# Kernel optimization log

Hardware: AMD Instinct MI355X
Metric: run time of the kernel (lower is better)

Reference implementation:

```python
import jax, jax.numpy as jnp
import numpy as np

B, C, H, W = 8, 512, 56, 56
CI = C // 2  # inter_channels
EPS = 1e-5   # BatchNorm eps


def setup_inputs() -> dict:
    key = jax.random.key(0)
    ks = jax.random.split(key, 11)
    s = 0.02
    return {
        "x": jax.random.normal(ks[0], (B, C, H, W), jnp.float32),
        "theta_w": jax.random.normal(ks[1], (CI, C), jnp.float32) * s,
        "theta_b": jnp.zeros((CI,), jnp.float32),
        "phi_w": jax.random.normal(ks[2], (CI, C), jnp.float32) * s,
        "phi_b": jnp.zeros((CI,), jnp.float32),
        "g_w": jax.random.normal(ks[3], (CI, C), jnp.float32) * s,
        "g_b": jnp.zeros((CI,), jnp.float32),
        "w_w": jax.random.normal(ks[4], (C, CI), jnp.float32) * s,
        "w_b": jnp.zeros((C,), jnp.float32),
        "bn_gamma": jax.random.normal(ks[5], (C,), jnp.float32) * 0.1,
        "bn_beta": jax.random.normal(ks[6], (C,), jnp.float32) * 0.1,
    }


def reference(x, theta_w, theta_b, phi_w, phi_b, g_w, g_b, w_w, w_b, bn_gamma, bn_beta):
    b, c, h, w = x.shape
    n = h * w

    def proj(wt, bi):  # 1x1 conv -> [b, out, n]
        return (jnp.einsum('bchw,oc->bohw', x, wt) + bi[None, :, None, None]).reshape(b, -1, n)

    theta_x = proj(theta_w, theta_b).transpose(0, 2, 1)  # [b, n, ci]
    phi_x = proj(phi_w, phi_b)                           # [b, ci, n]
    g_x = proj(g_w, g_b).transpose(0, 2, 1)             # [b, n, ci]

    f = jnp.einsum('bnc,bcm->bnm', theta_x, phi_x)       # [b, n, n] unscaled scores
    f_div_c = jax.nn.softmax(f, axis=-1)
    y = jnp.einsum('bnm,bmc->bnc', f_div_c, g_x)         # [b, n, ci]
    y = y.transpose(0, 2, 1).reshape(b, -1, h, w)        # [b, ci, h, w]

    w_y = jnp.einsum('bchw,oc->bohw', y, w_w) + w_b[None, :, None, None]
    # BatchNorm2d (training mode, batch statistics over B,H,W per channel)
    mean = w_y.mean(axis=(0, 2, 3))
    var = w_y.var(axis=(0, 2, 3))
    w_y = (w_y - mean[None, :, None, None]) * jax.lax.rsqrt(var[None, :, None, None] + EPS)
    w_y = w_y * bn_gamma[None, :, None, None] + bn_beta[None, :, None, None]
    return w_y + x
```

## Files before the change

kernel.cpp:

```cpp
#include <hip/hip_runtime.h>
#include <hip/hip_bf16.h>


typedef unsigned short u16;
typedef unsigned int u32;
typedef __attribute__((ext_vector_type(8))) short short8;
typedef __attribute__((ext_vector_type(4))) float floatx4;

#define B_   8
#define C_   512
#define CI_  256
#define N_   3136
#define BN_  25088

__device__ __forceinline__ u16 f2b(float f) {
    return __builtin_bit_cast(u16, __float2bfloat16(f));
}
__device__ __forceinline__ float b2f(u16 u) {
    return __bfloat162float(__builtin_bit_cast(__hip_bfloat16, u));
}
__device__ __forceinline__ floatx4 mfma16(short8 a, short8 b, floatx4 c) {
    return __builtin_amdgcn_mfma_f32_16x16x32_bf16(a, b, c, 0, 0, 0);
}
__device__ __forceinline__ void gload_lds16(const u16* g, u16* l) {
    __builtin_amdgcn_global_load_lds(
        (const __attribute__((address_space(1))) u32*)g,
        (__attribute__((address_space(3))) u32*)l, 16, 0, 0);
}

__device__ __forceinline__ int block_flag(const void* x) {
    __shared__ int cnt_;
    if (threadIdx.x == 0) cnt_ = 0;
    __syncthreads();
    const u32* xw = (const u32*)x;
    int c = 0;
#pragma unroll
    for (int i = 0; i < 4; ++i) {
        u32 w = xw[threadIdx.x * 4 + i];
        u32 e = (w >> 7) & 0xFF;
        c += (e >= 118 && e <= 130) ? 1 : 0;
    }
    atomicAdd(&cnt_, c);
    __syncthreads();
    return (2 * cnt_ > 1024) ? 1 : 0;
}

__global__ __launch_bounds__(256) void convert_params(
    const void* __restrict__ x,
    const void* tw, const void* tb, const void* pw, const void* pb,
    const void* gw, const void* gbi, const void* ww, const void* wb,
    const void* gamma, const void* beta,
    u16* __restrict__ dst, float* __restrict__ stats)
{
    const int fl = block_flag(x);
    if (blockIdx.x == 0 && blockIdx.y == 0) {
        stats[threadIdx.x] = 0.f;
        stats[threadIdx.x + 256] = 0.f;
        stats[threadIdx.x + 512] = 0.f;
        stats[threadIdx.x + 768] = 0.f;
    }
    const void* srcs[10] = {tw, tb, pw, pb, gw, gbi, ww, wb, gamma, beta};
    const int ns[10] = {131072, 256, 131072, 256, 131072, 256, 131072, 512, 512, 512};
    int seg = blockIdx.y;
    int off = 0;
    for (int s = 0; s < 10; ++s) { if (s == seg) break; off += ns[s]; }
    const void* src = srcs[seg];
    int n = ns[seg];
    int i0 = (blockIdx.x * 256 + threadIdx.x) * 8;
    if (i0 >= n) return;
    u16* d = dst + off;
    for (int k = 0; k < 8; ++k) {
        int i = i0 + k;
        if (i < n)
            d[i] = fl ? ((const u16*)src)[i] : f2b(((const float*)src)[i]);
    }
}

__global__ __launch_bounds__(256) void transpose_x(
    const void* __restrict__ in, u16* __restrict__ out)
{
    const int fl = block_flag(in);
    __shared__ u16 tile[64][68];
    const int t = threadIdx.x;
    const long base = (long)blockIdx.z * (long)C_ * (long)N_;
    const int c0 = blockIdx.x * 64, r0 = blockIdx.y * 64;
    const int lr = t >> 3;
    const int lc = (t & 7) * 8;
#pragma unroll
    for (int j = 0; j < 2; ++j) {
        int rr = lr + 32 * j;
        long eoff = base + (long)(r0 + rr) * N_ + c0 + lc;
        u16 v[8] __attribute__((aligned(16)));
        if (fl) {
            const u16* pi = (const u16*)in + eoff;
            *(uint64_t*)&v[0] = *(const uint64_t*)pi;
            *(uint64_t*)&v[4] = *(const uint64_t*)(pi + 4);
        } else {
            const float* pi = (const float*)in + eoff;
            floatx4 a = *(const floatx4*)pi;
            floatx4 b4 = *(const floatx4*)(pi + 4);
#pragma unroll
            for (int k = 0; k < 4; ++k) { v[k] = f2b(a[k]); v[4 + k] = f2b(b4[k]); }
        }
        *(uint64_t*)&tile[rr][lc] = *(const uint64_t*)&v[0];
        *(uint64_t*)&tile[rr][lc + 4] = *(const uint64_t*)&v[4];
    }
    __syncthreads();
#pragma unroll
    for (int j = 0; j < 2; ++j) {
        int oc = lr + 32 * j;
        int ob = (t & 7) * 8;
        u16 vals[8] __attribute__((aligned(16)));
#pragma unroll
        for (int k = 0; k < 8; ++k) vals[k] = tile[ob + k][oc];
        u16* po = out + (long)blockIdx.z * N_ * C_ + (long)(c0 + oc) * C_ + r0 + ob;
        *(uint64_t*)po = *(const uint64_t*)vals;
        *(uint64_t*)(po + 4) = *(const uint64_t*)(vals + 4);
    }
}

__global__ __launch_bounds__(256, 3) void gemm_proj(
    const u16* __restrict__ A,
    const u16* __restrict__ BtBase,
    u16* __restrict__ OutBase,
    u16* __restrict__ gT,
    long ostride)
{
    __shared__ __attribute__((aligned(16))) u16 smem[16896];
    const int t = threadIdx.x;
    const int wave = t >> 6, lane = t & 63;
    const int q = lane >> 4, lx = lane & 15;
    const int m0 = blockIdx.x * 128;
    const int n0 = blockIdx.y * 128;
    const int zz = blockIdx.z;
    const u16* Bt = BtBase + (long)zz * 131328L;
    const u16* bias = Bt + 131072;

    auto As = [&](int buf, int rg) -> u16* { return smem + (buf * 8 + rg) * 512; };
    auto Bs = [&](int buf, int rg) -> u16* { return smem + 8192 + (buf * 8 + rg) * 512; };

    floatx4 zero4 = {0.f, 0.f, 0.f, 0.f};
    floatx4 acc[4][4];
#pragma unroll
    for (int i = 0; i < 4; ++i)
#pragma unroll
        for (int j = 0; j < 4; ++j) acc[i][j] = zero4;

    auto stage = [&](int buf, int k0) {
#pragma unroll
        for (int i = 0; i < 2; ++i) {
            int rg = wave * 2 + i;
            gload_lds16(A + (long)(m0 + rg * 16 + lx) * C_ + k0 + q * 8, As(buf, rg));
            gload_lds16(Bt + (long)(n0 + rg * 16 + lx) * C_ + k0 + q * 8, Bs(buf, rg));
        }
    };

    stage(0, 0);
    const int rg0 = (wave >> 1) * 4, cg0 = (wave & 1) * 4;
    for (int s = 0; s < C_ / 32; ++s) {
        const int buf = s & 1;
        __syncthreads();
        if (s + 1 < C_ / 32) stage(buf ^ 1, (s + 1) * 32);
        short8 af[4], bfr[4];
#pragma unroll
        for (int i = 0; i < 4; ++i)
            af[i] = *(const short8*)(As(buf, rg0 + i) + lane * 8);
#pragma unroll
        for (int j = 0; j < 4; ++j)
            bfr[j] = *(const short8*)(Bs(buf, cg0 + j) + lane * 8);
#pragma unroll
        for (int i = 0; i < 4; ++i)
#pragma unroll
            for (int j = 0; j < 4; ++j)
                acc[i][j] = mfma16(af[i], bfr[j], acc[i][j]);
    }

    const int wr = (wave >> 1) * 64, wc = (wave & 1) * 64;
    if (zz < 2) {
        u16* Out = OutBase + (long)zz * ostride;
#pragma unroll
        for (int j = 0; j < 4; ++j) {
            int col = n0 + wc + j * 16 + lx;
            float bv = b2f(bias[col]);
#pragma unroll
            for (int i = 0; i < 4; ++i)
#pragma unroll
                for (int r = 0; r < 4; ++r) {
                    int row = m0 + wr + i * 16 + q * 4 + r;
                    Out[(long)row * CI_ + col] = f2b(acc[i][j][r] + bv);
                }
        }
    } else {
        __syncthreads();
#pragma unroll
        for (int j = 0; j < 4; ++j) {
            int cl = wc + j * 16 + lx;
            float bv = b2f(bias[n0 + cl]);
#pragma unroll
            for (int i = 0; i < 4; ++i)
#pragma unroll
                for (int r = 0; r < 4; ++r)
                    smem[cl * 132 + wr + i * 16 + q * 4 + r] =
                        f2b(acc[i][j][r] + bv);
        }
        __syncthreads();
#pragma unroll
        for (int p = 0; p < 4; ++p) {
            int cc = (t >> 3) + p * 32;
            int nn0 = (t & 7) * 16;
            u16 vals[16] __attribute__((aligned(16)));
#pragma unroll
            for (int k = 0; k < 16; ++k) vals[k] = smem[cc * 132 + nn0 + k];
            int m = m0 + nn0;
            int bb = m / N_;
            int nn = m - bb * N_;
            u16* dst = gT + ((long)bb * CI_ + (n0 + cc)) * N_ + nn;
            *(short8*)dst = *(const short8*)&vals[0];
            *(short8*)(dst + 8) = *(const short8*)&vals[8];
        }
    }
}

__global__ __launch_bounds__(256, 2) void attn(
    const u16* __restrict__ theta,
    const u16* __restrict__ phi,
    const u16* __restrict__ gT,
    u16* __restrict__ yp0, u16* __restrict__ yp1,
    u16* __restrict__ yp2, u16* __restrict__ yp3,
    float* __restrict__ lpart)
{
    __shared__ __attribute__((aligned(16))) u16 psf[2][8][2][64][8];
    __shared__ __attribute__((aligned(16))) u16 gsf[2][16][64][8];
    __shared__ __attribute__((aligned(16))) u16 Ps[4][32][40];

    const int t = threadIdx.x;
    const int wave = t >> 6, lane = t & 63;
    const int q = lane >> 4, lx = lane & 15;
    const int b = blockIdx.y;
    const int z = blockIdx.z;
    const int n0w = blockIdx.x * 128 + wave * 32;
    const bool valid = n0w < N_;
    const u16* thb = theta + (long)b * N_ * CI_;
    const u16* phb = phi + (long)b * N_ * CI_;
    const u16* gb = gT + (long)b * CI_ * N_;

    short8 tf[2][8];
#pragma unroll
    for (int h = 0; h < 2; ++h) {
        int trow = n0w + h * 16 + lx;
        if (trow >= N_) trow = N_ - 1;
#pragma unroll
        for (int kk = 0; kk < 8; ++kk)
            tf[h][kk] = *(const short8*)(thb + (long)trow * CI_ + kk * 32 + q * 8);
    }

    floatx4 zero4 = {0.f, 0.f, 0.f, 0.f};
    floatx4 yacc[2][16];
#pragma unroll
    for (int h = 0; h < 2; ++h)
#pragma unroll
        for (int i = 0; i < 16; ++i) yacc[h][i] = zero4;
    floatx4 lacc[2] = {zero4, zero4};
    const short8 ones = {0x3F80, 0x3F80, 0x3F80, 0x3F80,
                         0x3F80, 0x3F80, 0x3F80, 0x3F80};

    const int mbeg = z * 800;
    const int mend = (z == 3) ? N_ : mbeg + 800;

    auto stage = [&](int buf, int m0) {
#pragma unroll
        for (int i = 0; i < 2; ++i) {
            int kc = wave * 2 + i;
#pragma unroll
            for (int h = 0; h < 2; ++h)
                gload_lds16(phb + (long)(m0 + h * 16 + lx) * CI_ + kc * 32 + q * 8,
                            &psf[buf][kc][h][0][0]);
        }
#pragma unroll
        for (int j4 = 0; j4 < 4; ++j4) {
            int ct = wave * 4 + j4;
            gload_lds16(gb + (long)(ct * 16 + lx) * N_ + m0 + q * 8,
                        &gsf[buf][ct][0][0]);
        }
    };

    stage(0, mbeg);
    const int NSTEP = (mend - mbeg) / 32;
    for (int s = 0; s < NSTEP; ++s) {
        const int buf = s & 1;
        __syncthreads();
        if (s + 1 < NSTEP) stage(buf ^ 1, mbeg + (s + 1) * 32);

        floatx4 sacc[2][2];
        sacc[0][0] = zero4; sacc[0][1] = zero4;
        sacc[1][0] = zero4; sacc[1][1] = zero4;
#pragma unroll
        for (int kk = 0; kk < 8; ++kk) {
            short8 bf0 = *(const short8*)&psf[buf][kk][0][lane][0];
            short8 bf1 = *(const short8*)&psf[buf][kk][1][lane][0];
            sacc[0][0] = mfma16(tf[0][kk], bf0, sacc[0][0]);
            sacc[1][0] = mfma16(tf[1][kk], bf0, sacc[1][0]);
            sacc[0][1] = mfma16(tf[0][kk], bf1, sacc[0][1]);
            sacc[1][1] = mfma16(tf[1][kk], bf1, sacc[1][1]);
        }

#pragma unroll
        for (int h = 0; h < 2; ++h)
#pragma unroll
            for (int mh = 0; mh < 2; ++mh)
#pragma unroll
                for (int r = 0; r < 4; ++r) {
                    float e = __expf(fminf(sacc[h][mh][r], 60.f));
                    Ps[wave][h * 16 + q * 4 + r][mh * 16 + lx] = f2b(e);
                }
        short8 gpre[4];
#pragma unroll
        for (int j = 0; j < 4; ++j)
            gpre[j] = *(const short8*)&gsf[buf][j][lane][0];
        __builtin_amdgcn_wave_barrier();
        short8 pA0 = *(const short8*)&Ps[wave][lx][q * 8];
        short8 pA1 = *(const short8*)&Ps[wave][16 + lx][q * 8];
        __builtin_amdgcn_wave_barrier();

#pragma unroll
        for (int j = 0; j < 4; ++j) {
            yacc[0][j] = mfma16(pA0, gpre[j], yacc[0][j]);
            yacc[1][j] = mfma16(pA1, gpre[j], yacc[1][j]);
        }
#pragma unroll
        for (int ct = 4; ct < 16; ++ct) {
            short8 gf = *(const short8*)&gsf[buf][ct][lane][0];
            yacc[0][ct] = mfma16(pA0, gf, yacc[0][ct]);
            yacc[1][ct] = mfma16(pA1, gf, yacc[1][ct]);
        }
        lacc[0] = mfma16(pA0, ones, lacc[0]);
        lacc[1] = mfma16(pA1, ones, lacc[1]);
    }

    if (valid) {
        u16* ypz = (z == 0) ? yp0 : (z == 1) ? yp1 : (z == 2) ? yp2 : yp3;
        u16* yb = ypz + (long)b * N_ * CI_;
#pragma unroll
        for (int h = 0; h < 2; ++h)
#pragma unroll
            for (int ct = 0; ct < 16; ++ct)
#pragma unroll
                for (int r = 0; r < 4; ++r)
                    yb[(long)(n0w + h * 16 + q * 4 + r) * CI_ + ct * 16 + lx] =
                        f2b(yacc[h][ct][r]);
        if (lx == 0) {
#pragma unroll
            for (int h = 0; h < 2; ++h)
#pragma unroll
                for (int r = 0; r < 4; ++r)
                    lpart[(long)z * BN_ + (long)b * N_ + n0w + h * 16 + q * 4 + r] =
                        lacc[h][r];
        }
    }
}

__global__ __launch_bounds__(256, 3) void gemm_w(
    const u16* __restrict__ yp0, const u16* __restrict__ yp1,
    const u16* __restrict__ yp2, const u16* __restrict__ yp3,
    const float* __restrict__ lpart,
    const u16* __restrict__ Bt,
    const u16* __restrict__ bias,
    u16* __restrict__ wy,
    float* __restrict__ stats)
{
    __shared__ __attribute__((aligned(16))) u16 Asf[2][8][64][8];
    __shared__ __attribute__((aligned(16))) u16 Bsf[2][8][64][8];

    const int t = threadIdx.x;
    const int wave = t >> 6, lane = t & 63;
    const int q = lane >> 4, lx = lane & 15;
    const int m0 = blockIdx.x * 128;
    const int n0 = blockIdx.y * 128;

    float rl[2];
#pragma unroll
    for (int i = 0; i < 2; ++i) {
        int row = m0 + (wave * 2 + i) * 16 + lx;
        rl[i] = 1.0f / (lpart[row] + lpart[BN_ + row] +
                        lpart[2 * BN_ + row] + lpart[3 * BN_ + row]);
    }

    floatx4 zero4 = {0.f, 0.f, 0.f, 0.f};
    floatx4 acc[4][4];
#pragma unroll
    for (int i = 0; i < 4; ++i)
#pragma unroll
        for (int j = 0; j < 4; ++j) acc[i][j] = zero4;

    short8 va[2][4];
    auto loadA = [&](int k0) {
#pragma unroll
        for (int i = 0; i < 2; ++i) {
            long off = (long)(m0 + (wave * 2 + i) * 16 + lx) * CI_ + k0 + q * 8;
            va[i][0] = *(const short8*)(yp0 + off);
            va[i][1] = *(const short8*)(yp1 + off);
            va[i][2] = *(const short8*)(yp2 + off);
            va[i][3] = *(const short8*)(yp3 + off);
        }
    };
    auto writeA = [&](int buf) {
#pragma unroll
        for (int i = 0; i < 2; ++i) {
            u16 pk[8] __attribute__((aligned(16)));
#pragma unroll
            for (int e = 0; e < 8; ++e) {
                float v = (b2f(((const u16*)&va[i][0])[e]) +
                           b2f(((const u16*)&va[i][1])[e]) +
                           b2f(((const u16*)&va[i][2])[e]) +
                           b2f(((const u16*)&va[i][3])[e])) * rl[i];
                pk[e] = f2b(v);
            }
            *(short8*)&Asf[buf][wave * 2 + i][lane][0] = *(const short8*)pk;
        }
    };
    auto stageB = [&](int buf, int k0) {
#pragma unroll
        for (int i = 0; i < 2; ++i) {
            int rg = wave * 2 + i;
            gload_lds16(Bt + (long)(n0 + rg * 16 + lx) * CI_ + k0 + q * 8,
                        &Bsf[buf][rg][0][0]);
        }
    };

    loadA(0); writeA(0); stageB(0, 0);
    const int rg0 = (wave >> 1) * 4, cg0 = (wave & 1) * 4;
    const int NS = CI_ / 32;
    for (int s = 0; s < NS; ++s) {
        const int buf = s & 1;
        __syncthreads();
        if (s + 1 < NS) { loadA((s + 1) * 32); stageB(buf ^ 1, (s + 1) * 32); }
        short8 af[4], bfr[4];
#pragma unroll
        for (int i = 0; i < 4; ++i)
            af[i] = *(const short8*)&Asf[buf][rg0 + i][lane][0];
#pragma unroll
        for (int j = 0; j < 4; ++j)
            bfr[j] = *(const short8*)&Bsf[buf][cg0 + j][lane][0];
#pragma unroll
        for (int i = 0; i < 4; ++i)
#pragma unroll
            for (int j = 0; j < 4; ++j)
                acc[i][j] = mfma16(af[i], bfr[j], acc[i][j]);
        if (s + 1 < NS) writeA(buf ^ 1);
    }

    const int wr = (wave >> 1) * 64, wc = (wave & 1) * 64;
#pragma unroll
    for (int j = 0; j < 4; ++j) {
        int col = n0 + wc + j * 16 + lx;
        float bv = b2f(bias[col]);
        float cs = 0.f, cq = 0.f;
#pragma unroll
        for (int i = 0; i < 4; ++i)
#pragma unroll
            for (int r = 0; r < 4; ++r) {
                int row = m0 + wr + i * 16 + q * 4 + r;
                float v = acc[i][j][r] + bv;
                wy[(long)row * C_ + col] = f2b(v);
                cs += v; cq += v * v;
            }
        cs += __shfl_xor(cs, 16); cs += __shfl_xor(cs, 32);
        cq += __shfl_xor(cq, 16); cq += __shfl_xor(cq, 32);
        if (q == 0) {
            atomicAdd(&stats[col], cs);
            atomicAdd(&stats[C_ + col], cq);
        }
    }
}

__global__ __launch_bounds__(256) void bn_apply(
    const u16* __restrict__ wy, const void* __restrict__ xv,
    const u16* __restrict__ gamma, const u16* __restrict__ beta,
    const float* __restrict__ stats, void* __restrict__ outv)
{
    const int fl = block_flag(xv);
    __shared__ float tile[64][65];
    const int t = threadIdx.x;
    const int nb0 = blockIdx.x * 64;
    const int c0 = blockIdx.y * 64;
    const int b = blockIdx.z;
#pragma unroll
    for (int j = 0; j < 4; ++j) {
        int row = (t >> 4) + 16 * j;
        int col = (t & 15) * 4;
        const u16* p = wy + ((long)b * N_ + nb0 + row) * C_ + c0 + col;
        u16 lv[4] __attribute__((aligned(8)));
        *(uint64_t*)lv = *(const uint64_t*)p;
#pragma unroll
        for (int k = 0; k < 4; ++k) tile[row][col + k] = b2f(lv[k]);
    }
    __syncthreads();
    const float inv = 1.0f / (float)BN_;
#pragma unroll
    for (int it = 0; it < 8; ++it) {
        int oc = (t >> 5) + 8 * it;
        int on = (t & 31) * 2;
        int c = c0 + oc;
        float mean = stats[c] * inv;
        float var = stats[C_ + c] * inv - mean * mean;
        float rstd = rsqrtf(var + 1e-5f);
        float sc = b2f(gamma[c]) * rstd;
        float sh = b2f(beta[c]) - mean * sc;
        long base = ((long)b * C_ + c) * N_ + nb0 + on;
        float v0 = tile[on][oc] * sc + sh;
        float v1 = tile[on + 1][oc] * sc + sh;
        if (fl) {
            v0 += b2f(((const u16*)xv)[base]);
            v1 += b2f(((const u16*)xv)[base + 1]);
            ((u16*)outv)[base] = f2b(v0);
            ((u16*)outv)[base + 1] = f2b(v1);
        } else {
            v0 += ((const float*)xv)[base];
            v1 += ((const float*)xv)[base + 1];
            ((float*)outv)[base] = v0;
            ((float*)outv)[base + 1] = v1;
        }
    }
}

extern "C" void kernel_launch(void* const* d_in, const int* in_sizes, int n_in,
                              void* d_out, int out_size, void* d_ws, size_t ws_size,
                              hipStream_t stream)
{
    (void)in_sizes; (void)n_in; (void)out_size; (void)ws_size;

    const size_t S = 12845056;
    const size_t SE = S / 2;
    char* base = (char*)d_ws;
    u16*   xT    = (u16*)(base);
    u16*   yp3   = (u16*)(base);
    u16*   yp2   = (u16*)(base + S);
    u16*   th    = (u16*)(base + 2 * S);
    u16*   wy    = (u16*)(base + 2 * S);
    u16*   gT    = (u16*)(base + 4 * S);
    float* lpart = (float*)(base + 5 * S);
    float* stats = (float*)(base + 5 * S + (size_t)4 * BN_ * 4);
    u16*   cw    = (u16*)(base + 5 * S + (size_t)4 * BN_ * 4 + 4096);

    u16* ctw = cw;
    u16* cww = cw + 393984;
    u16* cwb = cw + 525056;
    u16* cga = cw + 525568;
    u16* cbe = cw + 526080;

    u16* yp0 = (u16*)d_out;
    u16* yp1 = (u16*)d_out + SE;

    convert_params<<<dim3(64, 10), 256, 0, stream>>>(
        d_in[0], d_in[1], d_in[2], d_in[3], d_in[4], d_in[5], d_in[6],
        d_in[7], d_in[8], d_in[9], d_in[10], cw, stats);

    transpose_x<<<dim3(N_ / 64, C_ / 64, B_), 256, 0, stream>>>(d_in[0], xT);

    gemm_proj<<<dim3(BN_ / 128, CI_ / 128, 3), 256, 0, stream>>>(
        xT, ctw, th, gT, (long)SE);

    attn<<<dim3(25, B_, 4), 256, 0, stream>>>(
        th, th + SE, gT, yp0, yp1, yp2, yp3, lpart);

    gemm_w<<<dim3(BN_ / 128, C_ / 128), 256, 0, stream>>>(
        yp0, yp1, yp2, yp3, lpart, cww, cwb, wy, stats);

    bn_apply<<<dim3(N_ / 64, C_ / 64, B_), 256, 0, stream>>>(
        wy, d_in[0], cga, cbe, stats, d_out);
}
```

Baseline: 375.1 us.

## Transpose softmax tile in registers via permlane swaps instead of LDS round-trip

Swaps the MFMA operand order so the score accumulator comes out transposed, then packs the exponentials to bf16 with v_cvt_pk_bf16_f32 and rearranges them across lanes with v_permlane32/16_swap. This produces the A-operand for the P·G MFMA directly in registers, removing the per-wave LDS scratch buffer, its writes and reads, and the wave barriers. It also raises wave priority around the MFMA blocks with s_setprio. The lane permutation must exactly match the MFMA operand layout, so the change depends on CDNA-specific instructions.

```diff
diff --git a/kernel.cpp b/kernel.cpp
--- a/kernel.cpp
+++ b/kernel.cpp
@@ -6,6 +6,7 @@
 typedef unsigned int u32;
 typedef __attribute__((ext_vector_type(8))) short short8;
 typedef __attribute__((ext_vector_type(4))) float floatx4;
+typedef __attribute__((ext_vector_type(4))) u32 uint4v;
 
 #define B_   8
 #define C_   512
@@ -231,7 +232,6 @@
 {
     __shared__ __attribute__((aligned(16))) u16 psf[2][8][2][64][8];
     __shared__ __attribute__((aligned(16))) u16 gsf[2][16][64][8];
-    __shared__ __attribute__((aligned(16))) u16 Ps[4][32][40];
 
     const int t = threadIdx.x;
     const int wave = t >> 6, lane = t & 63;
@@ -294,47 +294,53 @@
         floatx4 sacc[2][2];
         sacc[0][0] = zero4; sacc[0][1] = zero4;
         sacc[1][0] = zero4; sacc[1][1] = zero4;
+        __builtin_amdgcn_s_setprio(1);
 #pragma unroll
         for (int kk = 0; kk < 8; ++kk) {
             short8 bf0 = *(const short8*)&psf[buf][kk][0][lane][0];
             short8 bf1 = *(const short8*)&psf[buf][kk][1][lane][0];
-            sacc[0][0] = mfma16(tf[0][kk], bf0, sacc[0][0]);
-            sacc[1][0] = mfma16(tf[1][kk], bf0, sacc[1][0]);
-            sacc[0][1] = mfma16(tf[0][kk], bf1, sacc[0][1]);
-            sacc[1][1] = mfma16(tf[1][kk], bf1, sacc[1][1]);
-        }
-
-#pragma unroll
-        for (int h = 0; h < 2; ++h)
-#pragma unroll
-            for (int mh = 0; mh < 2; ++mh)
-#pragma unroll
-                for (int r = 0; r < 4; ++r) {
-                    float e = __expf(fminf(sacc[h][mh][r], 60.f));
-                    Ps[wave][h * 16 + q * 4 + r][mh * 16 + lx] = f2b(e);
-                }
-        short8 gpre[4];
-#pragma unroll
-        for (int j = 0; j < 4; ++j)
-            gpre[j] = *(const short8*)&gsf[buf][j][lane][0];
-        __builtin_amdgcn_wave_barrier();
-        short8 pA0 = *(const short8*)&Ps[wave][lx][q * 8];
-        short8 pA1 = *(const short8*)&Ps[wave][16 + lx][q * 8];
-        __builtin_amdgcn_wave_barrier();
-
-#pragma unroll
-        for (int j = 0; j < 4; ++j) {
-            yacc[0][j] = mfma16(pA0, gpre[j], yacc[0][j]);
-            yacc[1][j] = mfma16(pA1, gpre[j], yacc[1][j]);
-        }
-#pragma unroll
-        for (int ct = 4; ct < 16; ++ct) {
+            sacc[0][0] = mfma16(bf0, tf[0][kk], sacc[0][0]);
+            sacc[1][0] = mfma16(bf0, tf[1][kk], sacc[1][0]);
+            sacc[0][1] = mfma16(bf1, tf[0][kk], sacc[0][1]);
+            sacc[1][1] = mfma16(bf1, tf[1][kk], sacc[1][1]);
+        }
+        __builtin_amdgcn_s_setprio(0);
+
+        short8 pA[2];
+#pragma unroll
+        for (int h = 0; h < 2; ++h) {
+            float e0 = __expf(fminf(sacc[h][0][0], 60.f));
+            float e1 = __expf(fminf(sacc[h][0][1], 60.f));
+            float e2 = __expf(fminf(sacc[h][0][2], 60.f));
+            float e3 = __expf(fminf(sacc[h][0][3], 60.f));
+            float f0 = __expf(fminf(sacc[h][1][0], 60.f));
+            float f1 = __expf(fminf(sacc[h][1][1], 60.f));
+            float f2 = __expf(fminf(sacc[h][1][2], 60.f));
+            float f3 = __expf(fminf(sacc[h][1][3], 60.f));
+            u32 A0, A1, B0, B1;
+            asm("v_cvt_pk_bf16_f32 %0, %1, %2" : "=v"(A0) : "v"(e0), "v"(e1));
+            asm("v_cvt_pk_bf16_f32 %0, %1, %2" : "=v"(A1) : "v"(e2), "v"(e3));
+            asm("v_cvt_pk_bf16_f32 %0, %1, %2" : "=v"(B0) : "v"(f0), "v"(f1));
+            asm("v_cvt_pk_bf16_f32 %0, %1, %2" : "=v"(B1) : "v"(f2), "v"(f3));
+            asm("v_permlane32_swap_b32 %0, %1" : "+v"(A0), "+v"(B0));
+            asm("v_permlane32_swap_b32 %0, %1" : "+v"(A1), "+v"(B1));
+            asm("v_permlane16_swap_b32 %0, %1" : "+v"(A0), "+v"(B0));
+            asm("v_permlane16_swap_b32 %0, %1" : "+v"(A1), "+v"(B1));
+            uint4v pk;
+            pk[0] = A0; pk[1] = A1; pk[2] = B0; pk[3] = B1;
+            pA[h] = __builtin_bit_cast(short8, pk);
+        }
+
+        __builtin_amdgcn_s_setprio(1);
+#pragma unroll
+        for (int ct = 0; ct < 16; ++ct) {
             short8 gf = *(const short8*)&gsf[buf][ct][lane][0];
-            yacc[0][ct] = mfma16(pA0, gf, yacc[0][ct]);
-            yacc[1][ct] = mfma16(pA1, gf, yacc[1][ct]);
-        }
-        lacc[0] = mfma16(pA0, ones, lacc[0]);
-        lacc[1] = mfma16(pA1, ones, lacc[1]);
+            yacc[0][ct] = mfma16(pA[0], gf, yacc[0][ct]);
+            yacc[1][ct] = mfma16(pA[1], gf, yacc[1][ct]);
+        }
+        lacc[0] = mfma16(pA[0], ones, lacc[0]);
+        lacc[1] = mfma16(pA[1], ones, lacc[1]);
+        __builtin_amdgcn_s_setprio(0);
     }
 
     if (valid) {
```

Measured after the change: 372.6 us (median of 2 runs). About the same (-0.6%).
